# Kernel optimization log

Hardware: AMD Instinct MI355X
Metric: run time of the kernel (lower is better)

## Reference

```python
import jax, jax.numpy as jnp
import numpy as np

NUM_CLASSES = 100000
FEAT_DIM = 128
BATCH = 16384
LOSS_WEIGHT = 0.01


def setup_inputs() -> dict:
    key = jax.random.key(0)
    k1, k2, k3 = jax.random.split(key, 3)
    y = jax.random.randint(k1, (BATCH,), 0, NUM_CLASSES, dtype=jnp.int64)
    feat = jax.random.normal(k2, (BATCH, FEAT_DIM), dtype=jnp.float32)
    centers = jax.random.normal(k3, (NUM_CLASSES, FEAT_DIM), dtype=jnp.float32)
    return {"y": y, "feat": feat, "centers": centers}


def reference(y, feat, centers):
    # hist: per-class counts (torch.histc with unit-width bins over [0, num_classes])
    counts = jax.ops.segment_sum(jnp.ones((feat.shape[0],), feat.dtype), y,
                                 num_segments=NUM_CLASSES)  # [C]
    # per-class mean of features; zeros for empty classes (sum is 0 there)
    feat_sum = jax.ops.segment_sum(feat, y, num_segments=NUM_CLASSES)  # [C, D]
    feat_mean = feat_sum / jnp.maximum(counts, 1.0)[:, None]
    ratio = counts / (1.0 + counts)  # hist / (1 + hist)
    centers_grad = ratio[:, None] * (centers - feat_mean)  # [C, D]
    diff = feat - centers[y]  # gather centers per sample
    loss = LOSS_WEIGHT * 0.5 * jnp.sum(diff * diff)
    return (loss, centers_grad)
```

## Files before the change

kernel.cpp:

```cpp
#include <hip/hip_runtime.h>


#define BATCH   16384
#define FEAT    128
#define NCLASS  100000
#define LOSS_W  0.01f
#define CAP     32

__global__ __launch_bounds__(256)
void k_loss_hist(const int* __restrict__ y,
                 const float* __restrict__ feat,
                 const float* __restrict__ centers,
                 int* __restrict__ cnt,
                 int* __restrict__ bucket,
                 float* __restrict__ loss) {
    int t  = blockIdx.x * 256 + threadIdx.x;
    int i  = t >> 5;
    int d4 = (t & 31) << 2;
    int c  = y[i];

    const float4 f  = *(const float4*)(feat    + (size_t)i * FEAT + d4);
    const float4 ce = *(const float4*)(centers + (size_t)c * FEAT + d4);

    if (d4 == 0) {
        int r = atomicAdd(cnt + c, 1);
        if (r < CAP) bucket[(size_t)c * CAP + r] = i;
    }

    float dx = f.x - ce.x, dy = f.y - ce.y, dz = f.z - ce.z, dw = f.w - ce.w;
    float s = dx*dx + dy*dy + dz*dz + dw*dw;

    #pragma unroll
    for (int off = 32; off > 0; off >>= 1)
        s += __shfl_down(s, off, 64);

    __shared__ float smem[4];
    int lane = threadIdx.x & 63, wave = threadIdx.x >> 6;
    if (lane == 0) smem[wave] = s;
    __syncthreads();
    if (threadIdx.x == 0)
        atomicAdd(loss, LOSS_W * 0.5f * (smem[0] + smem[1] + smem[2] + smem[3]));
}

__global__ __launch_bounds__(256)
void k_grad(const float* __restrict__ centers,
            const int* __restrict__ cnt,
            const int* __restrict__ bucket,
            const float* __restrict__ feat,
            float* __restrict__ grad) {
    int wid  = (blockIdx.x * 256 + threadIdx.x) >> 6;
    int lane = threadIdx.x & 63;
    int c    = wid * 2 + (lane >> 5);
    int q    = lane & 31;
    if (c >= NCLASS) return;

    int n = cnt[c];
    float4* g = (float4*)(grad + (size_t)c * FEAT) + q;

    if (n == 0) {
        *g = make_float4(0.0f, 0.0f, 0.0f, 0.0f);
        return;
    }

    int m = n < CAP ? n : CAP;
    float4 acc = make_float4(0.0f, 0.0f, 0.0f, 0.0f);
    for (int k = 0; k < m; k++) {
        int i = bucket[(size_t)c * CAP + k];
        float4 f = *((const float4*)(feat + (size_t)i * FEAT) + q);
        acc.x += f.x; acc.y += f.y; acc.z += f.z; acc.w += f.w;
    }
    const float4 ce = *((const float4*)(centers + (size_t)c * FEAT) + q);

    float inv   = 1.0f / (float)n;
    float ratio = (float)n / (1.0f + (float)n);
    float4 o;
    o.x = ratio * (ce.x - acc.x * inv);
    o.y = ratio * (ce.y - acc.y * inv);
    o.z = ratio * (ce.z - acc.z * inv);
    o.w = ratio * (ce.w - acc.w * inv);
    *g = o;
}

extern "C" void kernel_launch(void* const* d_in, const int* in_sizes, int n_in,
                              void* d_out, int out_size, void* d_ws, size_t ws_size,
                              hipStream_t stream) {
    const int*   y       = (const int*)d_in[0];
    const float* feat    = (const float*)d_in[1];
    const float* centers = (const float*)d_in[2];

    float* loss = (float*)d_out;
    float* grad = (float*)d_out + 1;

    int* cnt    = (int*)d_ws;
    int* bucket = cnt + NCLASS;

    hipMemsetAsync(cnt, 0, (size_t)NCLASS * sizeof(int), stream);
    hipMemsetAsync(loss, 0, sizeof(float), stream);

    k_loss_hist<<<(BATCH * (FEAT / 4)) / 256, 256, 0, stream>>>(
        y, feat, centers, cnt, bucket, loss);

    k_grad<<<(NCLASS / 2 + 3) / 4, 256, 0, stream>>>(
        centers, cnt, bucket, feat, grad);
}
```

Measured before the change: 143.8 us.

## Compact occupied classes and zero gradient via memset instead of per-class kernel

The histogram kernel now records each newly occupied class in a compact list. The grad kernel launches one wave per occupied class, skipping empty classes, whose zero gradients come from a memset of the output buffer. This avoids reading centers and cnt for the many empty classes. In exchange it adds a global atomic counter and writes the occupied rows twice (memset, then kernel).

```diff
diff --git a/kernel.cpp b/kernel.cpp
--- a/kernel.cpp
+++ b/kernel.cpp
@@ -12,6 +12,8 @@
                  const float* __restrict__ feat,
                  const float* __restrict__ centers,
                  int* __restrict__ cnt,
+                 int* __restrict__ nocc,
+                 int* __restrict__ occ,
                  int* __restrict__ bucket,
                  float* __restrict__ loss) {
     int t  = blockIdx.x * 256 + threadIdx.x;
@@ -25,6 +27,7 @@
     if (d4 == 0) {
         int r = atomicAdd(cnt + c, 1);
         if (r < CAP) bucket[(size_t)c * CAP + r] = i;
+        if (r == 0) occ[atomicAdd(nocc, 1)] = c;
     }
 
     float dx = f.x - ce.x, dy = f.y - ce.y, dz = f.z - ce.z, dw = f.w - ce.w;
@@ -43,42 +46,34 @@
 }
 
 __global__ __launch_bounds__(256)
-void k_grad(const float* __restrict__ centers,
-            const int* __restrict__ cnt,
-            const int* __restrict__ bucket,
-            const float* __restrict__ feat,
-            float* __restrict__ grad) {
-    int wid  = (blockIdx.x * 256 + threadIdx.x) >> 6;
+void k_grad_occ(const float* __restrict__ centers,
+                const int* __restrict__ cnt,
+                const int* __restrict__ nocc,
+                const int* __restrict__ occ,
+                const int* __restrict__ bucket,
+                const float* __restrict__ feat,
+                float* __restrict__ grad) {
+    int w    = (blockIdx.x * 256 + threadIdx.x) >> 6;
     int lane = threadIdx.x & 63;
-    int c    = wid * 2 + (lane >> 5);
-    int q    = lane & 31;
-    if (c >= NCLASS) return;
+    if (w >= *nocc) return;
 
+    int c = occ[w];
     int n = cnt[c];
-    float4* g = (float4*)(grad + (size_t)c * FEAT) + q;
-
-    if (n == 0) {
-        *g = make_float4(0.0f, 0.0f, 0.0f, 0.0f);
-        return;
-    }
+    const float2 ce = *((const float2*)(centers + (size_t)c * FEAT) + lane);
 
     int m = n < CAP ? n : CAP;
-    float4 acc = make_float4(0.0f, 0.0f, 0.0f, 0.0f);
+    float ax = 0.0f, ay = 0.0f;
     for (int k = 0; k < m; k++) {
         int i = bucket[(size_t)c * CAP + k];
-        float4 f = *((const float4*)(feat + (size_t)i * FEAT) + q);
-        acc.x += f.x; acc.y += f.y; acc.z += f.z; acc.w += f.w;
+        float2 f = *((const float2*)(feat + (size_t)i * FEAT) + lane);
+        ax += f.x; ay += f.y;
     }
-    const float4 ce = *((const float4*)(centers + (size_t)c * FEAT) + q);
-
     float inv   = 1.0f / (float)n;
     float ratio = (float)n / (1.0f + (float)n);
-    float4 o;
-    o.x = ratio * (ce.x - acc.x * inv);
-    o.y = ratio * (ce.y - acc.y * inv);
-    o.z = ratio * (ce.z - acc.z * inv);
-    o.w = ratio * (ce.w - acc.w * inv);
-    *g = o;
+    float2 o;
+    o.x = ratio * (ce.x - ax * inv);
+    o.y = ratio * (ce.y - ay * inv);
+    *((float2*)(grad + (size_t)c * FEAT) + lane) = o;
 }
 
 extern "C" void kernel_launch(void* const* d_in, const int* in_sizes, int n_in,
@@ -92,14 +87,16 @@
     float* grad = (float*)d_out + 1;
 
     int* cnt    = (int*)d_ws;
-    int* bucket = cnt + NCLASS;
+    int* nocc   = cnt + NCLASS;
+    int* occ    = nocc + 1;
+    int* bucket = occ + BATCH;
 
-    hipMemsetAsync(cnt, 0, (size_t)NCLASS * sizeof(int), stream);
-    hipMemsetAsync(loss, 0, sizeof(float), stream);
+    hipMemsetAsync(d_out, 0, (size_t)out_size * sizeof(float), stream);
+    hipMemsetAsync(cnt, 0, (size_t)(NCLASS + 1) * sizeof(int), stream);
 
     k_loss_hist<<<(BATCH * (FEAT / 4)) / 256, 256, 0, stream>>>(
-        y, feat, centers, cnt, bucket, loss);
+        y, feat, centers, cnt, nocc, occ, bucket, loss);
 
-    k_grad<<<(NCLASS / 2 + 3) / 4, 256, 0, stream>>>(
-        centers, cnt, bucket, feat, grad);
+    k_grad_occ<<<BATCH / 4, 256, 0, stream>>>(
+        centers, cnt, nocc, occ, bucket, feat, grad);
 }
```

New measurement: 219.4 us. 52.6% more time.

## Fuse loss computation into per-class gradient pass with deterministic partial reduction

Applied to the files above, without the earlier changes.

The histogram pass now only reads labels, and the squared-distance loss moves into the per-class gradient kernel. That kernel already loads each sample's features and its class center, so feat and centers are not read a second time. Loss partials are written per block and summed by a single-block final kernel, replacing a global float atomic and a memset. This adds a third launch, and loss is computed only from bucketed samples, so any class with more than CAP members would drop terms from the loss.

```diff
diff --git a/kernel.cpp b/kernel.cpp
--- a/kernel.cpp
+++ b/kernel.cpp
@@ -6,79 +6,81 @@
 #define NCLASS  100000
 #define LOSS_W  0.01f
 #define CAP     32
+#define NPART   12500
 
 __global__ __launch_bounds__(256)
-void k_loss_hist(const int* __restrict__ y,
-                 const float* __restrict__ feat,
-                 const float* __restrict__ centers,
-                 int* __restrict__ cnt,
-                 int* __restrict__ bucket,
-                 float* __restrict__ loss) {
-    int t  = blockIdx.x * 256 + threadIdx.x;
-    int i  = t >> 5;
-    int d4 = (t & 31) << 2;
-    int c  = y[i];
-
-    const float4 f  = *(const float4*)(feat    + (size_t)i * FEAT + d4);
-    const float4 ce = *(const float4*)(centers + (size_t)c * FEAT + d4);
-
-    if (d4 == 0) {
-        int r = atomicAdd(cnt + c, 1);
-        if (r < CAP) bucket[(size_t)c * CAP + r] = i;
-    }
-
-    float dx = f.x - ce.x, dy = f.y - ce.y, dz = f.z - ce.z, dw = f.w - ce.w;
-    float s = dx*dx + dy*dy + dz*dz + dw*dw;
-
-    #pragma unroll
-    for (int off = 32; off > 0; off >>= 1)
-        s += __shfl_down(s, off, 64);
-
-    __shared__ float smem[4];
-    int lane = threadIdx.x & 63, wave = threadIdx.x >> 6;
-    if (lane == 0) smem[wave] = s;
-    __syncthreads();
-    if (threadIdx.x == 0)
-        atomicAdd(loss, LOSS_W * 0.5f * (smem[0] + smem[1] + smem[2] + smem[3]));
+void k_hist(const int* __restrict__ y,
+            int* __restrict__ cnt,
+            int* __restrict__ bucket) {
+    int i = blockIdx.x * 256 + threadIdx.x;
+    int c = y[i];
+    int r = atomicAdd(cnt + c, 1);
+    if (r < CAP) bucket[c * CAP + r] = i;
 }
 
 __global__ __launch_bounds__(256)
-void k_grad(const float* __restrict__ centers,
-            const int* __restrict__ cnt,
-            const int* __restrict__ bucket,
-            const float* __restrict__ feat,
-            float* __restrict__ grad) {
+void k_grad_loss(const float* __restrict__ centers,
+                 const int* __restrict__ cnt,
+                 const int* __restrict__ bucket,
+                 const float* __restrict__ feat,
+                 float* __restrict__ grad,
+                 float* __restrict__ partial) {
     int wid  = (blockIdx.x * 256 + threadIdx.x) >> 6;
     int lane = threadIdx.x & 63;
     int c    = wid * 2 + (lane >> 5);
     int q    = lane & 31;
-    if (c >= NCLASS) return;
+    int n = cnt[c];
 
-    int n = cnt[c];
-    float4* g = (float4*)(grad + (size_t)c * FEAT) + q;
-
-    if (n == 0) {
-        *g = make_float4(0.0f, 0.0f, 0.0f, 0.0f);
-        return;
-    }
+    float4 ce = make_float4(0.0f, 0.0f, 0.0f, 0.0f);
+    if (n > 0)
+        ce = *((const float4*)(centers + (size_t)c * FEAT) + q);
 
     int m = n < CAP ? n : CAP;
     float4 acc = make_float4(0.0f, 0.0f, 0.0f, 0.0f);
+    float ls = 0.0f;
     for (int k = 0; k < m; k++) {
-        int i = bucket[(size_t)c * CAP + k];
+        int i = bucket[c * CAP + k];
         float4 f = *((const float4*)(feat + (size_t)i * FEAT) + q);
         acc.x += f.x; acc.y += f.y; acc.z += f.z; acc.w += f.w;
+        float dx = f.x - ce.x, dy = f.y - ce.y;
+        float dz = f.z - ce.z, dw = f.w - ce.w;
+        ls += dx*dx + dy*dy + dz*dz + dw*dw;
     }
-    const float4 ce = *((const float4*)(centers + (size_t)c * FEAT) + q);
 
-    float inv   = 1.0f / (float)n;
-    float ratio = (float)n / (1.0f + (float)n);
-    float4 o;
-    o.x = ratio * (ce.x - acc.x * inv);
-    o.y = ratio * (ce.y - acc.y * inv);
-    o.z = ratio * (ce.z - acc.z * inv);
-    o.w = ratio * (ce.w - acc.w * inv);
-    *g = o;
+    float4 o = make_float4(0.0f, 0.0f, 0.0f, 0.0f);
+    if (n > 0) {
+        float inv   = 1.0f / (float)n;
+        float ratio = (float)n / (1.0f + (float)n);
+        o.x = ratio * (ce.x - acc.x * inv);
+        o.y = ratio * (ce.y - acc.y * inv);
+        o.z = ratio * (ce.z - acc.z * inv);
+        o.w = ratio * (ce.w - acc.w * inv);
+    }
+    *((float4*)(grad + (size_t)c * FEAT) + q) = o;
+
+    #pragma unroll
+    for (int off = 32; off > 0; off >>= 1)
+        ls += __shfl_down(ls, off, 64);
+    __shared__ float smem[4];
+    if (lane == 0) smem[threadIdx.x >> 6] = ls;
+    __syncthreads();
+    if (threadIdx.x == 0)
+        partial[blockIdx.x] = smem[0] + smem[1] + smem[2] + smem[3];
+}
+
+__global__ __launch_bounds__(256)
+void k_loss_final(const float* __restrict__ partial,
+                  float* __restrict__ loss) {
+    float s = 0.0f;
+    for (int i = threadIdx.x; i < NPART; i += 256) s += partial[i];
+    #pragma unroll
+    for (int off = 32; off > 0; off >>= 1)
+        s += __shfl_down(s, off, 64);
+    __shared__ float smem[4];
+    if ((threadIdx.x & 63) == 0) smem[threadIdx.x >> 6] = s;
+    __syncthreads();
+    if (threadIdx.x == 0)
+        *loss = LOSS_W * 0.5f * (smem[0] + smem[1] + smem[2] + smem[3]);
 }
 
 extern "C" void kernel_launch(void* const* d_in, const int* in_sizes, int n_in,
@@ -91,15 +93,16 @@
     float* loss = (float*)d_out;
     float* grad = (float*)d_out + 1;
 
-    int* cnt    = (int*)d_ws;
-    int* bucket = cnt + NCLASS;
+    int*   cnt     = (int*)d_ws;
+    int*   bucket  = cnt + NCLASS;
+    float* partial = (float*)(bucket + (size_t)NCLASS * CAP);
 
     hipMemsetAsync(cnt, 0, (size_t)NCLASS * sizeof(int), stream);
-    hipMemsetAsync(loss, 0, sizeof(float), stream);
 
-    k_loss_hist<<<(BATCH * (FEAT / 4)) / 256, 256, 0, stream>>>(
-        y, feat, centers, cnt, bucket, loss);
+    k_hist<<<BATCH / 256, 256, 0, stream>>>(y, cnt, bucket);
 
-    k_grad<<<(NCLASS / 2 + 3) / 4, 256, 0, stream>>>(
-        centers, cnt, bucket, feat, grad);
+    k_grad_loss<<<NPART, 256, 0, stream>>>(
+        centers, cnt, bucket, feat, grad, partial);
+
+    k_loss_final<<<1, 256, 0, stream>>>(partial, loss);
 }
```

Result: faster. 137.1 us (-4.7%).
